# Kernel optimization log

Hardware: AMD Instinct MI355X
Metric: run time of the kernel (lower is better)

The kernel has to match this reference:

```python
import jax, jax.numpy as jnp
import numpy as np

EPS = 1e-6

def _rms(x, g):
    # RMSNorm over last dim (head_dim)
    return x * jax.lax.rsqrt(jnp.mean(x * x, axis=-1, keepdims=True) + EPS) * g

def _split_heads(x, h):
    b, l, hd = x.shape
    return x.reshape(b, l, h, hd // h).transpose(0, 2, 1, 3)  # b h l d

def setup_inputs() -> dict:
    key = jax.random.key(0)
    ks = jax.random.split(key, 10)
    B, Limg, Lip, D, Dip, Temb = 1, 2048, 512, 3072, 1280, 1280
    return {
        "ip_hidden_states": jax.random.normal(ks[0], (B, Lip, Dip), jnp.float32),
        "img_query": jax.random.normal(ks[1], (B, Limg, D), jnp.float32),
        "img_key": jax.random.normal(ks[2], (B, Limg, D), jnp.float32),
        "img_value": jax.random.normal(ks[3], (B, Limg, D), jnp.float32),
        "t_emb": jax.random.normal(ks[4], (B, Temb), jnp.float32),
        "w_ada": jax.random.normal(ks[5], (2 * Dip, Temb), jnp.float32) * 0.02,
        "b_ada": jnp.zeros((2 * Dip,), jnp.float32),
        "w_k_ip": jax.random.normal(ks[6], (D, Dip), jnp.float32) * 0.02,
        "w_v_ip": jax.random.normal(ks[7], (D, Dip), jnp.float32) * 0.02,
        "g_q": jnp.ones((128,), jnp.float32),
        "g_k": jnp.ones((128,), jnp.float32),
        "g_ipk": jnp.ones((128,), jnp.float32),
        "n_heads": 24,
    }

def reference(ip_hidden_states, img_query, img_key, img_value, t_emb,
              w_ada, b_ada, w_k_ip, w_v_ip, g_q, g_k, g_ipk, n_heads):
    # AdaLayerNorm ('normal' mode): silu + linear -> shift/scale, LayerNorm (no affine)
    e = jax.nn.silu(t_emb) @ w_ada.T + b_ada              # [B, 2*Dip]
    shift, scale = jnp.split(e, 2, axis=1)
    mu = jnp.mean(ip_hidden_states, axis=-1, keepdims=True)
    var = jnp.var(ip_hidden_states, axis=-1, keepdims=True)
    xn = (ip_hidden_states - mu) * jax.lax.rsqrt(var + EPS)
    ip_norm = xn * (1.0 + scale[:, None]) + shift[:, None]  # [B, Lip, Dip]

    ip_key = ip_norm @ w_k_ip.T                            # [B, Lip, D]
    ip_value = ip_norm @ w_v_ip.T

    q = _split_heads(img_query, n_heads)                   # [B, H, Limg, d]
    k = _split_heads(img_key, n_heads)
    v = _split_heads(img_value, n_heads)
    ipk = _split_heads(ip_key, n_heads)                    # [B, H, Lip, d]
    ipv = _split_heads(ip_value, n_heads)

    q = _rms(q, g_q)
    k = _rms(k, g_k)
    ipk = _rms(ipk, g_ipk)

    key_all = jnp.concatenate([k, ipk], axis=2)            # [B, H, Limg+Lip, d]
    val_all = jnp.concatenate([v, ipv], axis=2)

    d = q.shape[-1]
    scores = jnp.einsum('bhqd,bhkd->bhqk', q, key_all) * (1.0 / np.sqrt(d))
    probs = jax.nn.softmax(scores, axis=-1)
    out = jnp.einsum('bhqk,bhkd->bhqd', probs, val_all)    # [B, H, Limg, d]

    b, h, l, dd = out.shape
    return out.transpose(0, 2, 1, 3).reshape(b, l, h * dd)
```

## Files before the change

kernel.cpp:

```cpp
#include <hip/hip_runtime.h>
#include <math.h>

#define H    24
#define Dh   128
#define LIMG 2048
#define LIP  512
#define DM   3072
#define DIP  1280
#define LK   2560
#define EPSF 1e-6f
#define SM_SCALE 0.08838834764831845f

typedef __attribute__((ext_vector_type(8))) short bf16x8;
typedef __attribute__((ext_vector_type(4))) float f32x4;

typedef const unsigned int __attribute__((address_space(1))) gu32;
typedef unsigned int __attribute__((address_space(3))) lu32;

static __device__ __forceinline__ unsigned short f2bf(float x) {
  union { float f; unsigned u; } v; v.f = x;
  unsigned r = v.u + 0x7fffu + ((v.u >> 16) & 1u);
  return (unsigned short)(r >> 16);
}

static __device__ __forceinline__ float bf2f(unsigned short b) {
  union { unsigned u; float f; } v; v.u = ((unsigned)b) << 16;
  return v.f;
}

__global__ __launch_bounds__(256) void ada_kernel(
    const float* __restrict__ t_emb, const float* __restrict__ w_ada,
    const float* __restrict__ b_ada, float* __restrict__ e) {
  int j = blockIdx.x;
  int tid = threadIdx.x;
  const float* wrow = w_ada + (long)j * DIP;
  float acc = 0.f;
  for (int k = tid; k < DIP; k += 256) {
    float t = t_emb[k];
    acc += (t / (1.f + expf(-t))) * wrow[k];
  }
#pragma unroll
  for (int m = 1; m < 64; m <<= 1) acc += __shfl_xor(acc, m, 64);
  __shared__ float red[4];
  if ((tid & 63) == 0) red[tid >> 6] = acc;
  __syncthreads();
  if (tid == 0) e[j] = red[0] + red[1] + red[2] + red[3] + b_ada[j];
}

__global__ __launch_bounds__(256) void adaln_kernel(
    const float* __restrict__ x, const float* __restrict__ e,
    unsigned short* __restrict__ ipnh, unsigned short* __restrict__ ipnl) {
  int r = blockIdx.x;
  int tid = threadIdx.x;
  const float* xr = x + (long)r * DIP;
  float v[5];
  float s = 0.f, ss = 0.f;
#pragma unroll
  for (int i = 0; i < 5; i++) {
    v[i] = xr[tid + i * 256];
    s += v[i];
    ss += v[i] * v[i];
  }
#pragma unroll
  for (int m = 1; m < 64; m <<= 1) {
    s += __shfl_xor(s, m, 64);
    ss += __shfl_xor(ss, m, 64);
  }
  __shared__ float rs_[4], rss_[4];
  if ((tid & 63) == 0) { rs_[tid >> 6] = s; rss_[tid >> 6] = ss; }
  __syncthreads();
  s = rs_[0] + rs_[1] + rs_[2] + rs_[3];
  ss = rss_[0] + rss_[1] + rss_[2] + rss_[3];
  float mu = s * (1.f / DIP);
  float var = ss * (1.f / DIP) - mu * mu;
  float rstd = rsqrtf(var + EPSF);
  unsigned short* oh = ipnh + (long)r * DIP;
  unsigned short* ol = ipnl + (long)r * DIP;
#pragma unroll
  for (int i = 0; i < 5; i++) {
    int c = tid + i * 256;
    float o = (v[i] - mu) * rstd * (1.f + e[DIP + c]) + e[c];
    unsigned short hb = f2bf(o);
    oh[c] = hb;
    ol[c] = f2bf(o - bf2f(hb));
  }
}

__global__ __launch_bounds__(256) void prep_kernel(
    const float* __restrict__ k_in, const float* __restrict__ v_in,
    const float* __restrict__ g_k,
    unsigned short* __restrict__ Kb, unsigned short* __restrict__ Vt) {
  __shared__ unsigned short Vls[128][33];
  int h = blockIdx.y, l0 = blockIdx.x * 32;
  int tid = threadIdx.x;
  int r = tid >> 3, c = tid & 7;
  const float* ksrc = k_in + (long)(l0 + r) * DM + h * Dh + c * 16;
  const float* vsrc = v_in + (long)(l0 + r) * DM + h * Dh + c * 16;
  float kv[16], vv[16];
  float ssq = 0.f;
#pragma unroll
  for (int i = 0; i < 4; i++) {
    float4 a = *(const float4*)(ksrc + i * 4);
    float4 b = *(const float4*)(vsrc + i * 4);
    kv[i*4+0]=a.x; kv[i*4+1]=a.y; kv[i*4+2]=a.z; kv[i*4+3]=a.w;
    vv[i*4+0]=b.x; vv[i*4+1]=b.y; vv[i*4+2]=b.z; vv[i*4+3]=b.w;
    ssq += a.x*a.x + a.y*a.y + a.z*a.z + a.w*a.w;
  }
  ssq += __shfl_xor(ssq, 1, 8);
  ssq += __shfl_xor(ssq, 2, 8);
  ssq += __shfl_xor(ssq, 4, 8);
  float rstd = rsqrtf(ssq * (1.f / Dh) + EPSF);
  unsigned short kb[16];
#pragma unroll
  for (int i = 0; i < 16; i++) kb[i] = f2bf(kv[i] * rstd * g_k[c * 16 + i]);
  unsigned short* kdst = Kb + ((long)h * LK + l0 + r) * Dh + c * 16;
  *(uint4*)(kdst) = *(uint4*)(kb);
  *(uint4*)(kdst + 8) = *(uint4*)(kb + 8);
#pragma unroll
  for (int i = 0; i < 16; i++) Vls[c * 16 + i][r] = f2bf(vv[i]);
  __syncthreads();
  int d = tid >> 1, half = (tid & 1) * 16;
  unsigned short ov[16];
#pragma unroll
  for (int j = 0; j < 16; j++) ov[j] = Vls[d][half + j];
  unsigned short* vdst = Vt + ((long)h * Dh + d) * LK + l0 + half;
  *(uint4*)(vdst) = *(uint4*)(ov);
  *(uint4*)(vdst + 8) = *(uint4*)(ov + 8);
}

__global__ __launch_bounds__(256) void proj_kernel(
    const unsigned short* __restrict__ Ah, const unsigned short* __restrict__ Al,
    const float* __restrict__ Wk, const float* __restrict__ Wv,
    const float* __restrict__ g_ipk,
    unsigned short* __restrict__ Kb, unsigned short* __restrict__ Vt) {
  __shared__ __align__(16) unsigned short lds[12288];
  unsigned short* Ahs = lds;
  unsigned short* Als = lds + 2048;
  unsigned short* Whs = lds + 4096;
  unsigned short* Wls = lds + 8192;
  const float* W = blockIdx.z ? Wv : Wk;
  int h = blockIdx.y;
  int m0 = blockIdx.x * 64;
  int tid = threadIdx.x;
  int w = tid >> 6, lane = tid & 63;
  int m = lane & 15, quad = lane >> 4;

  const float* wrow = W + (long)(h * Dh + (tid & 127)) * DIP + ((tid >> 7) << 3);
  const unsigned short* garow_h = Ah + (long)(m0 + lane) * DIP + w * 8;
  const unsigned short* garow_l = Al + (long)(m0 + lane) * DIP + w * 8;

  f32x4 acc[8];
#pragma unroll
  for (int i = 0; i < 8; i++) acc[i] = (f32x4){0.f, 0.f, 0.f, 0.f};

  float4 wa = *(const float4*)(wrow);
  float4 wb = *(const float4*)(wrow + 4);
  float4 wc = *(const float4*)(wrow + 16);
  float4 wd = *(const float4*)(wrow + 20);

#pragma unroll 1
  for (int k0 = 0; k0 < DIP; k0 += 32) {
    float cur[16] = {wa.x, wa.y, wa.z, wa.w, wb.x, wb.y, wb.z, wb.w,
                     wc.x, wc.y, wc.z, wc.w, wd.x, wd.y, wd.z, wd.w};
    if (k0 + 32 < DIP) {
      wa = *(const float4*)(wrow + k0 + 32);
      wb = *(const float4*)(wrow + k0 + 36);
      wc = *(const float4*)(wrow + k0 + 48);
      wd = *(const float4*)(wrow + k0 + 52);
    }
    unsigned short hi[16], lo[16];
#pragma unroll
    for (int i = 0; i < 16; i++) {
      unsigned short hb = f2bf(cur[i]);
      hi[i] = hb;
      lo[i] = f2bf(cur[i] - bf2f(hb));
    }
    __syncthreads();
    __builtin_amdgcn_global_load_lds((gu32*)(garow_h + k0), (lu32*)(Ahs + w * 512), 16, 0, 0);
    __builtin_amdgcn_global_load_lds((gu32*)(garow_l + k0), (lu32*)(Als + w * 512), 16, 0, 0);
    *(uint4*)(Whs + tid * 8) = *(uint4*)(hi);
    *(uint4*)(Wls + tid * 8) = *(uint4*)(lo);
    *(uint4*)(Whs + (tid + 256) * 8) = *(uint4*)(hi + 8);
    *(uint4*)(Wls + (tid + 256) * 8) = *(uint4*)(lo + 8);
    __syncthreads();

    bf16x8 ahf = *(const bf16x8*)(Ahs + ((quad << 6) + (w << 4) + m) * 8);
    bf16x8 alf = *(const bf16x8*)(Als + ((quad << 6) + (w << 4) + m) * 8);
#pragma unroll
    for (int nt = 0; nt < 8; nt++) {
      bf16x8 bhf = *(const bf16x8*)(Whs + ((quad << 7) + (nt << 4) + m) * 8);
      bf16x8 blf = *(const bf16x8*)(Wls + ((quad << 7) + (nt << 4) + m) * 8);
      acc[nt] = __builtin_amdgcn_mfma_f32_16x16x32_bf16(ahf, bhf, acc[nt], 0, 0, 0);
      acc[nt] = __builtin_amdgcn_mfma_f32_16x16x32_bf16(ahf, blf, acc[nt], 0, 0, 0);
      acc[nt] = __builtin_amdgcn_mfma_f32_16x16x32_bf16(alf, bhf, acc[nt], 0, 0, 0);
    }
  }

  if (blockIdx.z == 0) {
    float gkv[8];
#pragma unroll
    for (int nt = 0; nt < 8; nt++) gkv[nt] = g_ipk[nt * 16 + m];
#pragma unroll
    for (int r = 0; r < 4; r++) {
      float ssq = 0.f;
#pragma unroll
      for (int nt = 0; nt < 8; nt++) ssq += acc[nt][r] * acc[nt][r];
      ssq += __shfl_xor(ssq, 1, 16);
      ssq += __shfl_xor(ssq, 2, 16);
      ssq += __shfl_xor(ssq, 4, 16);
      ssq += __shfl_xor(ssq, 8, 16);
      float rstd = rsqrtf(ssq * (1.f / Dh) + EPSF);
      long row = (long)h * LK + LIMG + m0 + w * 16 + quad * 4 + r;
#pragma unroll
      for (int nt = 0; nt < 8; nt++)
        Kb[row * Dh + nt * 16 + m] = f2bf(acc[nt][r] * rstd * gkv[nt]);
    }
  } else {
#pragma unroll
    for (int nt = 0; nt < 8; nt++) {
      ushort4 o;
      o.x = f2bf(acc[nt][0]); o.y = f2bf(acc[nt][1]);
      o.z = f2bf(acc[nt][2]); o.w = f2bf(acc[nt][3]);
      *(ushort4*)(Vt + ((long)h * Dh + nt * 16 + m) * LK + LIMG + m0 + w * 16 + quad * 4) = o;
    }
  }
}

__global__ __launch_bounds__(256, 4) void flash_kernel(
    const float* __restrict__ q_in, const float* __restrict__ g_q,
    const unsigned short* __restrict__ Kb, const unsigned short* __restrict__ Vt,
    float* __restrict__ out) {
  __shared__ __align__(16) unsigned char lds[8192 + 8192 + 5120];
  unsigned short* Ks = (unsigned short*)lds;
  unsigned short* Vs = (unsigned short*)(lds + 8192);
  unsigned short* Ps = (unsigned short*)(lds + 16384);
  int tid = threadIdx.x;
  int w = tid >> 6, lid = tid & 63;
  int m = lid & 15, quad = lid >> 4;
  int h = blockIdx.y;
  int q0 = blockIdx.x * 64;
  int qrow = q0 + w * 16 + m;

  bf16x8 aq[4];
  {
    float qf[4][8];
    float ssq = 0.f;
    const float* qsrc = q_in + (long)qrow * DM + h * Dh + quad * 8;
#pragma unroll
    for (int ks = 0; ks < 4; ks++) {
      float4 a = *(const float4*)(qsrc + ks * 32);
      float4 b = *(const float4*)(qsrc + ks * 32 + 4);
      qf[ks][0]=a.x; qf[ks][1]=a.y; qf[ks][2]=a.z; qf[ks][3]=a.w;
      qf[ks][4]=b.x; qf[ks][5]=b.y; qf[ks][6]=b.z; qf[ks][7]=b.w;
      ssq += a.x*a.x + a.y*a.y + a.z*a.z + a.w*a.w;
      ssq += b.x*b.x + b.y*b.y + b.z*b.z + b.w*b.w;
    }
    ssq += __shfl_xor(ssq, 16, 64);
    ssq += __shfl_xor(ssq, 32, 64);
    float rstd = rsqrtf(ssq * (1.f / Dh) + EPSF);
    const float* gq = g_q + quad * 8;
#pragma unroll
    for (int ks = 0; ks < 4; ks++) {
      float4 ga = *(const float4*)(gq + ks * 32);
      float4 gb = *(const float4*)(gq + ks * 32 + 4);
      float gg[8] = {ga.x, ga.y, ga.z, ga.w, gb.x, gb.y, gb.z, gb.w};
#pragma unroll
      for (int j = 0; j < 8; j++)
        aq[ks][j] = (short)f2bf(qf[ks][j] * rstd * gg[j]);
    }
  }

  const unsigned short* KbH = Kb + (long)h * LK * Dh;
  const unsigned short* VtH = Vt + (long)h * Dh * LK;
  unsigned short* Pw = Ps + w * (16 * 40);

  f32x4 acc_o[8];
#pragma unroll
  for (int i = 0; i < 8; i++) acc_o[i] = (f32x4){0.f, 0.f, 0.f, 0.f};
  float mrun[4] = {-INFINITY, -INFINITY, -INFINITY, -INFINITY};
  float lrun[4] = {0.f, 0.f, 0.f, 0.f};

#pragma unroll 1
  for (int j0 = 0; j0 < LK; j0 += 32) {
    __syncthreads();
    {
      int sbase = w * 128;
#pragma unroll
      for (int is = 0; is < 2; is++) {
        int s = sbase + is * 64 + lid;
        int r = s >> 4, cc = s & 15;
        int c = cc ^ (r & 15);
        const unsigned short* g = KbH + (long)(j0 + r) * Dh + c * 8;
        __builtin_amdgcn_global_load_lds((gu32*)g, (lu32*)(Ks + (sbase + is * 64) * 8),
                                         16, 0, 0);
      }
#pragma unroll
      for (int is = 0; is < 2; is++) {
        int s = sbase + is * 64 + lid;
        int d = s >> 2, cc = s & 3;
        const unsigned short* g = VtH + (long)d * LK + j0 + cc * 8;
        __builtin_amdgcn_global_load_lds((gu32*)g, (lu32*)(Vs + (sbase + is * 64) * 8),
                                         16, 0, 0);
      }
    }
    __syncthreads();

    f32x4 sc[2];
    sc[0] = (f32x4){0.f, 0.f, 0.f, 0.f};
    sc[1] = (f32x4){0.f, 0.f, 0.f, 0.f};
#pragma unroll
    for (int t = 0; t < 2; t++)
#pragma unroll
      for (int ks = 0; ks < 4; ks++) {
        int rr = t * 16 + m;
        int g = (ks * 4 + quad) ^ m;
        bf16x8 bk = *(const bf16x8*)(Ks + rr * 128 + g * 8);
        sc[t] = __builtin_amdgcn_mfma_f32_16x16x32_bf16(aq[ks], bk, sc[t], 0, 0, 0);
      }

    float mx[4], al[4], ps0[4], ps1[4];
#pragma unroll
    for (int r = 0; r < 4; r++) {
      float v0 = sc[0][r] * SM_SCALE, v1 = sc[1][r] * SM_SCALE;
      ps0[r] = v0; ps1[r] = v1;
      float mm = fmaxf(v0, v1);
      mm = fmaxf(mm, __shfl_xor(mm, 1, 16));
      mm = fmaxf(mm, __shfl_xor(mm, 2, 16));
      mm = fmaxf(mm, __shfl_xor(mm, 4, 16));
      mm = fmaxf(mm, __shfl_xor(mm, 8, 16));
      mx[r] = mm;
    }
#pragma unroll
    for (int r = 0; r < 4; r++) {
      float mn = fmaxf(mrun[r], mx[r]);
      al[r] = __expf(mrun[r] - mn);
      mrun[r] = mn;
      float p0 = __expf(ps0[r] - mn), p1 = __expf(ps1[r] - mn);
      ps0[r] = p0; ps1[r] = p1;
      float s2 = p0 + p1;
      s2 += __shfl_xor(s2, 1, 16);
      s2 += __shfl_xor(s2, 2, 16);
      s2 += __shfl_xor(s2, 4, 16);
      s2 += __shfl_xor(s2, 8, 16);
      lrun[r] = lrun[r] * al[r] + s2;
    }
#pragma unroll
    for (int r = 0; r < 4; r++) {
      Pw[(quad * 4 + r) * 40 + m] = f2bf(ps0[r]);
      Pw[(quad * 4 + r) * 40 + 16 + m] = f2bf(ps1[r]);
    }
    __threadfence_block();
    bf16x8 ap = *(const bf16x8*)(Pw + m * 40 + quad * 8);
#pragma unroll
    for (int dt = 0; dt < 8; dt++) {
      acc_o[dt][0] *= al[0]; acc_o[dt][1] *= al[1];
      acc_o[dt][2] *= al[2]; acc_o[dt][3] *= al[3];
    }
#pragma unroll
    for (int dt = 0; dt < 8; dt++) {
      bf16x8 bv = *(const bf16x8*)(Vs + (dt * 16 + m) * 32 + quad * 8);
      acc_o[dt] = __builtin_amdgcn_mfma_f32_16x16x32_bf16(ap, bv, acc_o[dt], 0, 0, 0);
    }
  }

  float il[4] = {1.f / lrun[0], 1.f / lrun[1], 1.f / lrun[2], 1.f / lrun[3]};
#pragma unroll
  for (int dt = 0; dt < 8; dt++)
#pragma unroll
    for (int r = 0; r < 4; r++)
      out[(long)(q0 + w * 16 + quad * 4 + r) * DM + h * Dh + dt * 16 + m] =
          acc_o[dt][r] * il[r];
}

extern "C" void kernel_launch(void* const* d_in, const int* in_sizes, int n_in,
                              void* d_out, int out_size, void* d_ws, size_t ws_size,
                              hipStream_t stream) {
  const float* ip_hidden = (const float*)d_in[0];
  const float* img_q     = (const float*)d_in[1];
  const float* img_k     = (const float*)d_in[2];
  const float* img_v     = (const float*)d_in[3];
  const float* t_emb     = (const float*)d_in[4];
  const float* w_ada     = (const float*)d_in[5];
  const float* b_ada     = (const float*)d_in[6];
  const float* w_k_ip    = (const float*)d_in[7];
  const float* w_v_ip    = (const float*)d_in[8];
  const float* g_q       = (const float*)d_in[9];
  const float* g_k       = (const float*)d_in[10];
  const float* g_ipk     = (const float*)d_in[11];

  char* base = (char*)d_ws;
  float* e = (float*)base;
  unsigned short* ipnh = (unsigned short*)(base + 16384);
  unsigned short* ipnl = (unsigned short*)(base + 1327104);
  unsigned short* Kb   = (unsigned short*)(base + 2637824);
  unsigned short* Vt   = Kb + (size_t)H * LK * Dh;
  float* out = (float*)d_out;

  ada_kernel<<<2 * DIP, 256, 0, stream>>>(t_emb, w_ada, b_ada, e);
  adaln_kernel<<<LIP, 256, 0, stream>>>(ip_hidden, e, ipnh, ipnl);
  prep_kernel<<<dim3(LIMG / 32, H), 256, 0, stream>>>(img_k, img_v, g_k, Kb, Vt);
  proj_kernel<<<dim3(LIP / 64, H, 2), 256, 0, stream>>>(ipnh, ipnl, w_k_ip, w_v_ip,
                                                        g_ipk, Kb, Vt);
  flash_kernel<<<dim3(LIMG / 64, H), 256, 0, stream>>>(img_q, g_q, Kb, Vt, out);
}
```

Baseline: 451.0 us.

## Double-buffer K/V and weight staging, widen flash Q tile, swizzle V LDS

Both the projection and flash kernels now double-buffer their LDS staging. The next tile's global-to-LDS loads are issued before computing on the current tile, and one barrier per iteration is removed. The flash kernel now processes 128 query rows per block, two 16-row groups per wave, so each K/V tile staged in LDS is reused twice. It also uses a flat 384-block grid whose index interleaves heads, and an XOR swizzle on the V tile to avoid LDS bank conflicts. In exchange, LDS and register use roughly double, the occupancy hint drops to 2, and 384 blocks may fill the GPU unevenly.

```diff
diff --git a/kernel.cpp b/kernel.cpp
--- a/kernel.cpp
+++ b/kernel.cpp
@@ -133,11 +133,7 @@
     const float* __restrict__ Wk, const float* __restrict__ Wv,
     const float* __restrict__ g_ipk,
     unsigned short* __restrict__ Kb, unsigned short* __restrict__ Vt) {
-  __shared__ __align__(16) unsigned short lds[12288];
-  unsigned short* Ahs = lds;
-  unsigned short* Als = lds + 2048;
-  unsigned short* Whs = lds + 4096;
-  unsigned short* Wls = lds + 8192;
+  __shared__ __align__(16) unsigned short lds_u[24576];
   const float* W = blockIdx.z ? Wv : Wk;
   int h = blockIdx.y;
   int m0 = blockIdx.x * 64;
@@ -158,8 +154,7 @@
   float4 wc = *(const float4*)(wrow + 16);
   float4 wd = *(const float4*)(wrow + 20);
 
-#pragma unroll 1
-  for (int k0 = 0; k0 < DIP; k0 += 32) {
+  auto stagek = [&](int b, int k0) {
     float cur[16] = {wa.x, wa.y, wa.z, wa.w, wb.x, wb.y, wb.z, wb.w,
                      wc.x, wc.y, wc.z, wc.w, wd.x, wd.y, wd.z, wd.w};
     if (k0 + 32 < DIP) {
@@ -175,25 +170,40 @@
       hi[i] = hb;
       lo[i] = f2bf(cur[i] - bf2f(hb));
     }
-    __syncthreads();
-    __builtin_amdgcn_global_load_lds((gu32*)(garow_h + k0), (lu32*)(Ahs + w * 512), 16, 0, 0);
-    __builtin_amdgcn_global_load_lds((gu32*)(garow_l + k0), (lu32*)(Als + w * 512), 16, 0, 0);
-    *(uint4*)(Whs + tid * 8) = *(uint4*)(hi);
-    *(uint4*)(Wls + tid * 8) = *(uint4*)(lo);
-    *(uint4*)(Whs + (tid + 256) * 8) = *(uint4*)(hi + 8);
-    *(uint4*)(Wls + (tid + 256) * 8) = *(uint4*)(lo + 8);
-    __syncthreads();
-
-    bf16x8 ahf = *(const bf16x8*)(Ahs + ((quad << 6) + (w << 4) + m) * 8);
-    bf16x8 alf = *(const bf16x8*)(Als + ((quad << 6) + (w << 4) + m) * 8);
+    unsigned short* AhsB = lds_u + b * 12288;
+    unsigned short* AlsB = AhsB + 2048;
+    unsigned short* WhsB = AhsB + 4096;
+    unsigned short* WlsB = AhsB + 8192;
+    __builtin_amdgcn_global_load_lds((gu32*)(garow_h + k0), (lu32*)(AhsB + w * 512), 16, 0, 0);
+    __builtin_amdgcn_global_load_lds((gu32*)(garow_l + k0), (lu32*)(AlsB + w * 512), 16, 0, 0);
+    *(uint4*)(WhsB + tid * 8) = *(uint4*)(hi);
+    *(uint4*)(WlsB + tid * 8) = *(uint4*)(lo);
+    *(uint4*)(WhsB + (tid + 256) * 8) = *(uint4*)(hi + 8);
+    *(uint4*)(WlsB + (tid + 256) * 8) = *(uint4*)(lo + 8);
+  };
+
+  stagek(0, 0);
+  __syncthreads();
+  int buf = 0;
+#pragma unroll 1
+  for (int k0 = 0; k0 < DIP; k0 += 32) {
+    if (k0 + 32 < DIP) stagek(buf ^ 1, k0 + 32);
+    unsigned short* AhsB = lds_u + buf * 12288;
+    unsigned short* AlsB = AhsB + 2048;
+    unsigned short* WhsB = AhsB + 4096;
+    unsigned short* WlsB = AhsB + 8192;
+    bf16x8 ahf = *(const bf16x8*)(AhsB + ((quad << 6) + (w << 4) + m) * 8);
+    bf16x8 alf = *(const bf16x8*)(AlsB + ((quad << 6) + (w << 4) + m) * 8);
 #pragma unroll
     for (int nt = 0; nt < 8; nt++) {
-      bf16x8 bhf = *(const bf16x8*)(Whs + ((quad << 7) + (nt << 4) + m) * 8);
-      bf16x8 blf = *(const bf16x8*)(Wls + ((quad << 7) + (nt << 4) + m) * 8);
+      bf16x8 bhf = *(const bf16x8*)(WhsB + ((quad << 7) + (nt << 4) + m) * 8);
+      bf16x8 blf = *(const bf16x8*)(WlsB + ((quad << 7) + (nt << 4) + m) * 8);
       acc[nt] = __builtin_amdgcn_mfma_f32_16x16x32_bf16(ahf, bhf, acc[nt], 0, 0, 0);
       acc[nt] = __builtin_amdgcn_mfma_f32_16x16x32_bf16(ahf, blf, acc[nt], 0, 0, 0);
       acc[nt] = __builtin_amdgcn_mfma_f32_16x16x32_bf16(alf, bhf, acc[nt], 0, 0, 0);
     }
+    __syncthreads();
+    buf ^= 1;
   }
 
   if (blockIdx.z == 0) {
@@ -226,25 +236,28 @@
   }
 }
 
-__global__ __launch_bounds__(256, 4) void flash_kernel(
+__global__ __launch_bounds__(256, 2) void flash_kernel(
     const float* __restrict__ q_in, const float* __restrict__ g_q,
     const unsigned short* __restrict__ Kb, const unsigned short* __restrict__ Vt,
     float* __restrict__ out) {
-  __shared__ __align__(16) unsigned char lds[8192 + 8192 + 5120];
+  __shared__ __align__(16) unsigned char lds[16384 + 16384 + 10240];
   unsigned short* Ks = (unsigned short*)lds;
-  unsigned short* Vs = (unsigned short*)(lds + 8192);
-  unsigned short* Ps = (unsigned short*)(lds + 16384);
+  unsigned short* Vs = (unsigned short*)(lds + 16384);
+  unsigned short* Ps = (unsigned short*)(lds + 32768);
   int tid = threadIdx.x;
   int w = tid >> 6, lid = tid & 63;
   int m = lid & 15, quad = lid >> 4;
-  int h = blockIdx.y;
-  int q0 = blockIdx.x * 64;
-  int qrow = q0 + w * 16 + m;
-
-  bf16x8 aq[4];
-  {
+  int id = blockIdx.x;
+  int sidx = id >> 3;
+  int h = (id & 7) * 3 + (sidx >> 4);
+  int q0 = (sidx & 15) * 128;
+
+  bf16x8 aq[2][4];
+#pragma unroll
+  for (int g2 = 0; g2 < 2; g2++) {
     float qf[4][8];
     float ssq = 0.f;
+    int qrow = q0 + w * 32 + g2 * 16 + m;
     const float* qsrc = q_in + (long)qrow * DM + h * Dh + quad * 8;
 #pragma unroll
     for (int ks = 0; ks < 4; ks++) {
@@ -266,110 +279,131 @@
       float gg[8] = {ga.x, ga.y, ga.z, ga.w, gb.x, gb.y, gb.z, gb.w};
 #pragma unroll
       for (int j = 0; j < 8; j++)
-        aq[ks][j] = (short)f2bf(qf[ks][j] * rstd * gg[j]);
+        aq[g2][ks][j] = (short)f2bf(qf[ks][j] * rstd * gg[j]);
     }
   }
 
   const unsigned short* KbH = Kb + (long)h * LK * Dh;
   const unsigned short* VtH = Vt + (long)h * Dh * LK;
-  unsigned short* Pw = Ps + w * (16 * 40);
-
-  f32x4 acc_o[8];
-#pragma unroll
-  for (int i = 0; i < 8; i++) acc_o[i] = (f32x4){0.f, 0.f, 0.f, 0.f};
-  float mrun[4] = {-INFINITY, -INFINITY, -INFINITY, -INFINITY};
-  float lrun[4] = {0.f, 0.f, 0.f, 0.f};
-
+
+  f32x4 acc_o[2][8];
+#pragma unroll
+  for (int g2 = 0; g2 < 2; g2++)
+#pragma unroll
+    for (int i = 0; i < 8; i++) acc_o[g2][i] = (f32x4){0.f, 0.f, 0.f, 0.f};
+  float mrun[2][4] = {{-INFINITY,-INFINITY,-INFINITY,-INFINITY},
+                      {-INFINITY,-INFINITY,-INFINITY,-INFINITY}};
+  float lrun[2][4] = {{0.f,0.f,0.f,0.f},{0.f,0.f,0.f,0.f}};
+
+  auto stage = [&](int b, int j0) {
+    unsigned short* KsB = Ks + b * 4096;
+    unsigned short* VsB = Vs + b * 4096;
+    int sbase = w * 128;
+#pragma unroll
+    for (int is = 0; is < 2; is++) {
+      int s = sbase + is * 64 + lid;
+      int r = s >> 4, cc = s & 15;
+      int c = cc ^ (r & 15);
+      const unsigned short* g = KbH + (long)(j0 + r) * Dh + c * 8;
+      __builtin_amdgcn_global_load_lds((gu32*)g, (lu32*)(KsB + (sbase + is * 64) * 8),
+                                       16, 0, 0);
+    }
+#pragma unroll
+    for (int is = 0; is < 2; is++) {
+      int s = sbase + is * 64 + lid;
+      int d = s >> 2, cc = s & 3;
+      int c = cc ^ (d & 3);
+      const unsigned short* g = VtH + (long)d * LK + j0 + c * 8;
+      __builtin_amdgcn_global_load_lds((gu32*)g, (lu32*)(VsB + (sbase + is * 64) * 8),
+                                       16, 0, 0);
+    }
+  };
+
+  stage(0, 0);
+  __syncthreads();
+  int buf = 0;
 #pragma unroll 1
-  for (int j0 = 0; j0 < LK; j0 += 32) {
-    __syncthreads();
-    {
-      int sbase = w * 128;
-#pragma unroll
-      for (int is = 0; is < 2; is++) {
-        int s = sbase + is * 64 + lid;
-        int r = s >> 4, cc = s & 15;
-        int c = cc ^ (r & 15);
-        const unsigned short* g = KbH + (long)(j0 + r) * Dh + c * 8;
-        __builtin_amdgcn_global_load_lds((gu32*)g, (lu32*)(Ks + (sbase + is * 64) * 8),
-                                         16, 0, 0);
-      }
-#pragma unroll
-      for (int is = 0; is < 2; is++) {
-        int s = sbase + is * 64 + lid;
-        int d = s >> 2, cc = s & 3;
-        const unsigned short* g = VtH + (long)d * LK + j0 + cc * 8;
-        __builtin_amdgcn_global_load_lds((gu32*)g, (lu32*)(Vs + (sbase + is * 64) * 8),
-                                         16, 0, 0);
-      }
-    }
-    __syncthreads();
-
-    f32x4 sc[2];
-    sc[0] = (f32x4){0.f, 0.f, 0.f, 0.f};
-    sc[1] = (f32x4){0.f, 0.f, 0.f, 0.f};
+  for (int jt = 0; jt < LK / 32; ++jt) {
+    if (jt + 1 < LK / 32) stage(buf ^ 1, (jt + 1) * 32);
+    unsigned short* KsB = Ks + buf * 4096;
+    unsigned short* VsB = Vs + buf * 4096;
+
+    f32x4 sc[2][2];
+    sc[0][0] = (f32x4){0.f,0.f,0.f,0.f}; sc[0][1] = (f32x4){0.f,0.f,0.f,0.f};
+    sc[1][0] = (f32x4){0.f,0.f,0.f,0.f}; sc[1][1] = (f32x4){0.f,0.f,0.f,0.f};
 #pragma unroll
     for (int t = 0; t < 2; t++)
 #pragma unroll
       for (int ks = 0; ks < 4; ks++) {
         int rr = t * 16 + m;
         int g = (ks * 4 + quad) ^ m;
-        bf16x8 bk = *(const bf16x8*)(Ks + rr * 128 + g * 8);
-        sc[t] = __builtin_amdgcn_mfma_f32_16x16x32_bf16(aq[ks], bk, sc[t], 0, 0, 0);
+        bf16x8 bk = *(const bf16x8*)(KsB + rr * 128 + g * 8);
+        sc[0][t] = __builtin_amdgcn_mfma_f32_16x16x32_bf16(aq[0][ks], bk, sc[0][t], 0, 0, 0);
+        sc[1][t] = __builtin_amdgcn_mfma_f32_16x16x32_bf16(aq[1][ks], bk, sc[1][t], 0, 0, 0);
       }
 
-    float mx[4], al[4], ps0[4], ps1[4];
-#pragma unroll
-    for (int r = 0; r < 4; r++) {
-      float v0 = sc[0][r] * SM_SCALE, v1 = sc[1][r] * SM_SCALE;
-      ps0[r] = v0; ps1[r] = v1;
-      float mm = fmaxf(v0, v1);
-      mm = fmaxf(mm, __shfl_xor(mm, 1, 16));
-      mm = fmaxf(mm, __shfl_xor(mm, 2, 16));
-      mm = fmaxf(mm, __shfl_xor(mm, 4, 16));
-      mm = fmaxf(mm, __shfl_xor(mm, 8, 16));
-      mx[r] = mm;
-    }
-#pragma unroll
-    for (int r = 0; r < 4; r++) {
-      float mn = fmaxf(mrun[r], mx[r]);
-      al[r] = __expf(mrun[r] - mn);
-      mrun[r] = mn;
-      float p0 = __expf(ps0[r] - mn), p1 = __expf(ps1[r] - mn);
-      ps0[r] = p0; ps1[r] = p1;
-      float s2 = p0 + p1;
-      s2 += __shfl_xor(s2, 1, 16);
-      s2 += __shfl_xor(s2, 2, 16);
-      s2 += __shfl_xor(s2, 4, 16);
-      s2 += __shfl_xor(s2, 8, 16);
-      lrun[r] = lrun[r] * al[r] + s2;
-    }
-#pragma unroll
-    for (int r = 0; r < 4; r++) {
-      Pw[(quad * 4 + r) * 40 + m] = f2bf(ps0[r]);
-      Pw[(quad * 4 + r) * 40 + 16 + m] = f2bf(ps1[r]);
+    float al[2][4];
+#pragma unroll
+    for (int g2 = 0; g2 < 2; g2++) {
+      float mx[4], ps0[4], ps1[4];
+#pragma unroll
+      for (int r = 0; r < 4; r++) {
+        float v0 = sc[g2][0][r] * SM_SCALE, v1 = sc[g2][1][r] * SM_SCALE;
+        ps0[r] = v0; ps1[r] = v1;
+        float mm = fmaxf(v0, v1);
+        mm = fmaxf(mm, __shfl_xor(mm, 1, 16));
+        mm = fmaxf(mm, __shfl_xor(mm, 2, 16));
+        mm = fmaxf(mm, __shfl_xor(mm, 4, 16));
+        mm = fmaxf(mm, __shfl_xor(mm, 8, 16));
+        mx[r] = mm;
+      }
+      unsigned short* Pw = Ps + (w * 2 + g2) * 640;
+#pragma unroll
+      for (int r = 0; r < 4; r++) {
+        float mn = fmaxf(mrun[g2][r], mx[r]);
+        al[g2][r] = __expf(mrun[g2][r] - mn);
+        mrun[g2][r] = mn;
+        float p0 = __expf(ps0[r] - mn), p1 = __expf(ps1[r] - mn);
+        float s2 = p0 + p1;
+        s2 += __shfl_xor(s2, 1, 16);
+        s2 += __shfl_xor(s2, 2, 16);
+        s2 += __shfl_xor(s2, 4, 16);
+        s2 += __shfl_xor(s2, 8, 16);
+        lrun[g2][r] = lrun[g2][r] * al[g2][r] + s2;
+        Pw[(quad * 4 + r) * 40 + m] = f2bf(p0);
+        Pw[(quad * 4 + r) * 40 + 16 + m] = f2bf(p1);
+      }
     }
     __threadfence_block();
-    bf16x8 ap = *(const bf16x8*)(Pw + m * 40 + quad * 8);
+    bf16x8 ap0 = *(const bf16x8*)(Ps + (w * 2 + 0) * 640 + m * 40 + quad * 8);
+    bf16x8 ap1 = *(const bf16x8*)(Ps + (w * 2 + 1) * 640 + m * 40 + quad * 8);
+
 #pragma unroll
     for (int dt = 0; dt < 8; dt++) {
-      acc_o[dt][0] *= al[0]; acc_o[dt][1] *= al[1];
-      acc_o[dt][2] *= al[2]; acc_o[dt][3] *= al[3];
-    }
-#pragma unroll
-    for (int dt = 0; dt < 8; dt++) {
-      bf16x8 bv = *(const bf16x8*)(Vs + (dt * 16 + m) * 32 + quad * 8);
-      acc_o[dt] = __builtin_amdgcn_mfma_f32_16x16x32_bf16(ap, bv, acc_o[dt], 0, 0, 0);
-    }
-  }
-
-  float il[4] = {1.f / lrun[0], 1.f / lrun[1], 1.f / lrun[2], 1.f / lrun[3]};
-#pragma unroll
-  for (int dt = 0; dt < 8; dt++)
-#pragma unroll
-    for (int r = 0; r < 4; r++)
-      out[(long)(q0 + w * 16 + quad * 4 + r) * DM + h * Dh + dt * 16 + m] =
-          acc_o[dt][r] * il[r];
+      bf16x8 bv = *(const bf16x8*)(VsB + ((dt * 16 + m) * 4 + (quad ^ (m & 3))) * 8);
+#pragma unroll
+      for (int r = 0; r < 4; r++) {
+        acc_o[0][dt][r] *= al[0][r];
+        acc_o[1][dt][r] *= al[1][r];
+      }
+      acc_o[0][dt] = __builtin_amdgcn_mfma_f32_16x16x32_bf16(ap0, bv, acc_o[0][dt], 0, 0, 0);
+      acc_o[1][dt] = __builtin_amdgcn_mfma_f32_16x16x32_bf16(ap1, bv, acc_o[1][dt], 0, 0, 0);
+    }
+    __syncthreads();
+    buf ^= 1;
+  }
+
+#pragma unroll
+  for (int g2 = 0; g2 < 2; g2++) {
+    float il[4] = {1.f / lrun[g2][0], 1.f / lrun[g2][1],
+                   1.f / lrun[g2][2], 1.f / lrun[g2][3]};
+#pragma unroll
+    for (int dt = 0; dt < 8; dt++)
+#pragma unroll
+      for (int r = 0; r < 4; r++)
+        out[(long)(q0 + w * 32 + g2 * 16 + quad * 4 + r) * DM + h * Dh + dt * 16 + m] =
+            acc_o[g2][dt][r] * il[r];
+  }
 }
 
 extern "C" void kernel_launch(void* const* d_in, const int* in_sizes, int n_in,
@@ -401,5 +435,5 @@
   prep_kernel<<<dim3(LIMG / 32, H), 256, 0, stream>>>(img_k, img_v, g_k, Kb, Vt);
   proj_kernel<<<dim3(LIP / 64, H, 2), 256, 0, stream>>>(ipnh, ipnl, w_k_ip, w_v_ip,
                                                         g_ipk, Kb, Vt);
-  flash_kernel<<<dim3(LIMG / 64, H), 256, 0, stream>>>(img_q, g_q, Kb, Vt, out);
-}
+  flash_kernel<<<dim3(384), 256, 0, stream>>>(img_q, g_q, Kb, Vt, out);
+}
```

After: 498.3 us. 10.5% more time.
